# Performance work log

Hardware: AMD Instinct MI355X
Metric: run time of the kernel (lower is better)

The kernel has to match this reference:

```python
import jax, jax.numpy as jnp
import numpy as np

N = 150000   # total supergraph nodes (entities+events+chains)
D = 128      # embed_size
H = 4        # attention heads
DH = D // H  # head dim
E = 300000   # edges per layer
L = 4        # layer_specs length
A = 8        # edge attr dim
T = 10       # num_edge_type
TIME_SCALE = 24.0
SLOPE = 0.2  # negative_slope


def setup_inputs() -> dict:
    key = jax.random.key(0)
    ks = jax.random.split(key, 16)
    nrm = lambda k, s, sc=1.0: jax.random.normal(k, s, dtype=jnp.float32) * sc
    return {
        'x': nrm(ks[0], (N, D), 0.1),
        'Wq': nrm(ks[1], (L, D, D), D ** -0.5),
        'Wk': nrm(ks[2], (L, D, D), D ** -0.5),
        'Wv': nrm(ks[3], (L, D, D), D ** -0.5),
        'Wskip': nrm(ks[4], (L, D, D), D ** -0.5),
        'Wa': nrm(ks[5], (L, A, D), 0.1),
        'time_w': nrm(ks[6], (D,)),
        'time_b': nrm(ks[7], (D,), 0.1),
        'dist_w': nrm(ks[8], (D,)),
        'dist_b': nrm(ks[9], (D,), 0.1),
        'type_table': nrm(ks[10], (T, D), 0.1),
        'bn_gamma': jnp.ones((L, D), jnp.float32),
        'bn_beta': jnp.zeros((L, D), jnp.float32),
        'beta': jnp.full((L,), 0.5, jnp.float32),
        'edge_attr': jax.random.uniform(ks[11], (L, E, A), dtype=jnp.float32),
        'edge_dt': jax.random.uniform(ks[12], (L, E), dtype=jnp.float32) * TIME_SCALE,
        'edge_ds': jax.random.uniform(ks[13], (L, E), dtype=jnp.float32) * 10.0,
        'edge_index': jax.random.randint(ks[14], (L, 2, E), 0, N),
        'edge_type': jax.random.randint(ks[15], (L, E), 0, T),
    }


def _layer(x, Wq, Wk, Wv, Wskip, Wa, time_w, time_b, dist_w, dist_b,
           type_table, gamma, bvec, beta, attr, dt, ds, ei, et):
    n = x.shape[0]
    src, dst = ei[0], ei[1]
    # continuous time / distance encoders: cos basis (TimeEncoder / 'time' DistanceEncoder)
    te = jnp.cos((dt / TIME_SCALE)[:, None] * time_w + time_b)   # [E,D]
    de = jnp.cos(ds[:, None] * dist_w + dist_b)                  # [E,D]
    # 'add' edge/time fusion: attr MLP + time + dist + edge-type embeddings
    edge_feat = attr @ Wa + te + de + type_table[et]             # [E,D]
    kv_in = x[src] + edge_feat                                   # gather + fuse
    q = (x @ Wq).reshape(n, H, DH)[dst]                          # [E,H,DH]
    k = (kv_in @ Wk).reshape(-1, H, DH)
    v = (kv_in @ Wv).reshape(-1, H, DH)
    logits = (q * k).sum(-1) * (DH ** -0.5)                      # [E,H]
    logits = jnp.where(logits >= 0, logits, SLOPE * logits)      # leaky_relu(negative_slope)
    # segment softmax over incoming edges of each destination node
    m = jax.ops.segment_max(logits, dst, num_segments=n)
    a = jnp.exp(logits - m[dst])
    denom = jax.ops.segment_sum(a, dst, num_segments=n)
    a = a / denom[dst]
    agg = jax.ops.segment_sum(a[..., None] * v, dst, num_segments=n).reshape(n, D)
    # beta-weighted residual (learn_beta) with skip projection
    out = beta * (x @ Wskip) + (1.0 - beta) * agg
    # BatchNorm1d (training-mode batch stats) + ReLU
    mu = out.mean(0)
    var = out.var(0)
    out = (out - mu) * jax.lax.rsqrt(var + 1e-5) * gamma + bvec
    return jax.nn.relu(out)


def reference(x, Wq, Wk, Wv, Wskip, Wa, time_w, time_b, dist_w, dist_b,
              type_table, bn_gamma, bn_beta, beta, edge_attr, edge_dt,
              edge_ds, edge_index, edge_type):
    for l in range(L):  # entity2event, event2event, event2chain (time filter), chain2chain
        x = _layer(x, Wq[l], Wk[l], Wv[l], Wskip[l], Wa[l],
                   time_w, time_b, dist_w, dist_b, type_table,
                   bn_gamma[l], bn_beta[l], beta[l],
                   edge_attr[l], edge_dt[l], edge_ds[l],
                   edge_index[l], edge_type[l])
    return x
```

## Files before the change

### kernel.cpp

```cpp
#include <hip/hip_runtime.h>

typedef unsigned int u32;
typedef unsigned short u16;
typedef short bf16x8 __attribute__((ext_vector_type(8)));
typedef float f32x4 __attribute__((ext_vector_type(4)));

#define N_NODES 150000
#define E_EDGES 300000
#define L_CNT   151552
#define ETILES  9375
#define NTILES  4688
#define KVBLKS  37500
#define PREPB   42192
#define SCATB   2344

__device__ __forceinline__ float blo(u32 u){ return __uint_as_float(u << 16); }
__device__ __forceinline__ float bhi(u32 u){ return __uint_as_float(u & 0xffff0000u); }
__device__ __forceinline__ float b2f(u16 h){ return __uint_as_float(((u32)h) << 16); }
__device__ __forceinline__ u16 f2bf(float f){
  u32 u = __float_as_uint(f);
  return (u16)((u + 0x7fffu + ((u >> 16) & 1u)) >> 16);
}
__device__ __forceinline__ u32 pack2(float a, float b){
  return (u32)f2bf(a) | ((u32)f2bf(b) << 16);
}

__device__ __forceinline__ f32x4 mfma16(bf16x8 a, bf16x8 b, f32x4 c){
  return __builtin_amdgcn_mfma_f32_16x16x32_bf16(a, b, c, 0, 0, 0);
}

__device__ __forceinline__ int opsw(int r, int k){ return (r * 128 + k) ^ ((r & 7) << 3); }
__device__ __forceinline__ int csw(int r, int n){ return (r * 128 + n) ^ (((r >> 2) & 3) << 3); }

__global__ __launch_bounds__(256)
void k_wt(const float* __restrict__ Wq, const float* __restrict__ Wk,
          const float* __restrict__ Wv, const float* __restrict__ Ws,
          u16* __restrict__ Wt)
{
  const int m = blockIdx.x;
  const float* src = (m < 4 ? Wq : m < 8 ? Wk : m < 12 ? Wv : Ws)
                     + (size_t)(m & 3) * 16384;
  u16* dst = Wt + (size_t)m * 16384;
  const int t = threadIdx.x;
  for (int i = 0; i < 16; ++i) {
    int idx = i * 256 + t;
    int n = idx >> 5;
    int k4 = (idx & 31) << 2;
    ushort4 o;
    o.x = f2bf(src[(k4 + 0) * 128 + n]);
    o.y = f2bf(src[(k4 + 1) * 128 + n]);
    o.z = f2bf(src[(k4 + 2) * 128 + n]);
    o.w = f2bf(src[(k4 + 3) * 128 + n]);
    *(ushort4*)(dst + n * 128 + k4) = o;
  }
}


__global__ __launch_bounds__(256)
void k_hist(const int* __restrict__ eidx, int* __restrict__ counts)
{
  const int l = blockIdx.y;
  const int e = blockIdx.x * 256 + threadIdx.x;
  if (e < E_EDGES) {
    int dst = eidx[(size_t)l * 2 * E_EDGES + E_EDGES + e];
    atomicAdd(&counts[(size_t)l * L_CNT + dst], 1);
  }
}

__global__ __launch_bounds__(256)
void k_scan1(const int* __restrict__ counts, int* __restrict__ rowptr,
             int* __restrict__ bsum)
{
  __shared__ int sh[256];
  const int b = blockIdx.x, l = blockIdx.y;
  const int t = threadIdx.x;
  const int* c = counts + (size_t)l * L_CNT + b * 2048;
  int* rp = rowptr + (size_t)l * L_CNT + b * 2048;
  int v[8]; int s = 0;
  #pragma unroll
  for (int j = 0; j < 8; ++j) { v[j] = c[t * 8 + j]; s += v[j]; }
  sh[t] = s; __syncthreads();
  for (int off = 1; off < 256; off <<= 1) {
    int x = (t >= off) ? sh[t - off] : 0;
    __syncthreads();
    sh[t] += x;
    __syncthreads();
  }
  int excl = (t == 0) ? 0 : sh[t - 1];
  if (t == 255) bsum[l * 128 + b] = sh[255];
  int run = excl;
  #pragma unroll
  for (int j = 0; j < 8; ++j) { rp[t * 8 + j] = run; run += v[j]; }
}

__global__ __launch_bounds__(128)
void k_scan2(int* __restrict__ bsum)
{
  __shared__ int sh[128];
  const int l = blockIdx.x, t = threadIdx.x;
  int v = (t < 74) ? bsum[l * 128 + t] : 0;
  sh[t] = v; __syncthreads();
  for (int off = 1; off < 128; off <<= 1) {
    int x = (t >= off) ? sh[t - off] : 0;
    __syncthreads();
    sh[t] += x;
    __syncthreads();
  }
  int excl = (t == 0) ? 0 : sh[t - 1];
  if (t < 74) bsum[l * 128 + t] = excl;
}

__global__ __launch_bounds__(256)
void k_scan3(int* __restrict__ rowptr, int* __restrict__ tmp,
             const int* __restrict__ bsum)
{
  const int l = blockIdx.y;
  const int q = blockIdx.x * 256 + threadIdx.x;
  int v = rowptr[(size_t)l * L_CNT + q] + bsum[l * 128 + (q >> 11)];
  rowptr[(size_t)l * L_CNT + q] = v;
  tmp[(size_t)l * L_CNT + q] = v;
}

__device__ __forceinline__ void scatter_one(
    int e, const int* __restrict__ srcP, const int* __restrict__ dstP,
    const int* __restrict__ etP, const float* __restrict__ dtP,
    const float* __restrict__ dsP, const float* __restrict__ attrP,
    int* __restrict__ tmpL, u32* __restrict__ meta)
{
  int dst = dstP[e];
  int pos = atomicAdd(&tmpL[dst], 1);
  int src = srcP[e];
  int et  = etP[e];
  float dtn = dtP[e] * (1.0f / 24.0f);
  float dsv = dsP[e];
  float4 aA = *(const float4*)(attrP + (size_t)e * 8);
  float4 aB = *(const float4*)(attrP + (size_t)e * 8 + 4);
  uint4 r0, r1;
  r0.x = (u32)src;
  r0.y = (u32)dst | ((u32)et << 20);
  r0.z = __float_as_uint(dtn);
  r0.w = __float_as_uint(dsv);
  r1.x = pack2(aA.x, aA.y); r1.y = pack2(aA.z, aA.w);
  r1.z = pack2(aB.x, aB.y); r1.w = pack2(aB.z, aB.w);
  u32* mp = meta + (size_t)pos * 8;
  *(uint4*)mp = r0;
  *(uint4*)(mp + 4) = r1;
}

__global__ __launch_bounds__(256)
void k_scatter(const int* __restrict__ srcP, const int* __restrict__ dstP,
               const int* __restrict__ etP, const float* __restrict__ dtP,
               const float* __restrict__ dsP, const float* __restrict__ attrP,
               int* __restrict__ tmpL, u32* __restrict__ meta)
{
  const int e = blockIdx.x * 256 + threadIdx.x;
  if (e < E_EDGES)
    scatter_one(e, srcP, dstP, etP, dtP, dsP, attrP, tmpL, meta);
}

__global__ __launch_bounds__(128)
void bn_stats(const float* __restrict__ colsum, const float* __restrict__ colsumsq,
              const float* __restrict__ gamma, const float* __restrict__ bvec,
              float* __restrict__ scsh)
{
  const int d = threadIdx.x;
  const float invN = 1.f / 150000.f;
  float mu = colsum[d] * invN;
  float var = colsumsq[d] * invN - mu * mu;
  float sc = gamma[d] * rsqrtf(var + 1e-5f);
  scsh[d] = sc;
  scsh[128 + d] = bvec[d] - mu * sc;
}


template<int XF32, int BN>
__global__ __launch_bounds__(128, 2)
void prep(const void* __restrict__ xg, const u16* __restrict__ WtQ,
          const u16* __restrict__ WtS, const float* __restrict__ scsh,
          u16* __restrict__ Qo, u16* __restrict__ So,
          const float* __restrict__ Wa, const float* __restrict__ tw,
          const float* __restrict__ tb, const float* __restrict__ dw,
          const float* __restrict__ db, const float* __restrict__ ttab,
          const u32* __restrict__ meta, u16* __restrict__ kvV,
          const int* __restrict__ srcN, const int* __restrict__ dstN,
          const int* __restrict__ etN, const float* __restrict__ dtN,
          const float* __restrict__ dsN, const float* __restrict__ attrN,
          int* __restrict__ tmpN, u32* __restrict__ metaN)
{
  __shared__ __align__(16) u16 As[4160];
  __shared__ __align__(16) u16 Bs[4160];
  const int b = blockIdx.x;
  const int t = threadIdx.x;

  if (b >= PREPB) {
    int e = (b - PREPB) * 128 + t;
    if (metaN != nullptr && e < E_EDGES)
      scatter_one(e, srcN, dstN, etN, dtN, dsN, attrN, tmpN, metaN);
    return;
  }

  if (b % 9 == 0) {
    const int w = t >> 6, lane = t & 63;
    const int lr = lane & 15, hi = lane >> 4;
    const int row0 = (b / 9) * 32;
    const int nr = min(32, N_NODES - row0);
    const u16* Wt = w ? WtS : WtQ;
    u16* C = w ? So : Qo;

    bf16x8 wt[8][4];
    #pragma unroll
    for (int nb = 0; nb < 8; ++nb)
      #pragma unroll
      for (int ks = 0; ks < 4; ++ks)
        wt[nb][ks] = *(const bf16x8*)(Wt + (nb * 16 + lr) * 128 + ks * 32 + hi * 8);

    #pragma unroll
    for (int i = 0; i < 4; ++i) {
      int idx = i * 128 + t;
      int r = idx >> 4, c8 = (idx & 15) << 3;
      if (r < nr) {
        if (XF32) {
          float4 vA = *(const float4*)((const float*)xg + (size_t)(row0 + r) * 128 + c8);
          float4 vB = *(const float4*)((const float*)xg + (size_t)(row0 + r) * 128 + c8 + 4);
          uint4 o;
          o.x = pack2(vA.x, vA.y); o.y = pack2(vA.z, vA.w);
          o.z = pack2(vB.x, vB.y); o.w = pack2(vB.z, vB.w);
          *(uint4*)(As + opsw(r, c8)) = o;
        } else {
          uint4 v = *(const uint4*)((const u16*)xg + (size_t)(row0 + r) * 128 + c8);
          if (BN) {
            float4 scA = *(const float4*)(scsh + c8);
            float4 scB = *(const float4*)(scsh + c8 + 4);
            float4 shA = *(const float4*)(scsh + 128 + c8);
            float4 shB = *(const float4*)(scsh + 128 + c8 + 4);
            float e0v = fmaxf(fmaf(blo(v.x), scA.x, shA.x), 0.f);
            float e1v = fmaxf(fmaf(bhi(v.x), scA.y, shA.y), 0.f);
            float e2v = fmaxf(fmaf(blo(v.y), scA.z, shA.z), 0.f);
            float e3v = fmaxf(fmaf(bhi(v.y), scA.w, shA.w), 0.f);
            float e4v = fmaxf(fmaf(blo(v.z), scB.x, shB.x), 0.f);
            float e5v = fmaxf(fmaf(bhi(v.z), scB.y, shB.y), 0.f);
            float e6v = fmaxf(fmaf(blo(v.w), scB.z, shB.z), 0.f);
            float e7v = fmaxf(fmaf(bhi(v.w), scB.w, shB.w), 0.f);
            v.x = pack2(e0v, e1v); v.y = pack2(e2v, e3v);
            v.z = pack2(e4v, e5v); v.w = pack2(e6v, e7v);
          }
          *(uint4*)(As + opsw(r, c8)) = v;
        }
      } else {
        *(uint4*)(As + opsw(r, c8)) = make_uint4(0, 0, 0, 0);
      }
    }
    __syncthreads();

    f32x4 acc[2][8];
    #pragma unroll
    for (int a = 0; a < 2; ++a)
      #pragma unroll
      for (int bb = 0; bb < 8; ++bb) {
        acc[a][bb][0] = 0.f; acc[a][bb][1] = 0.f;
        acc[a][bb][2] = 0.f; acc[a][bb][3] = 0.f;
      }
    #pragma unroll
    for (int ks = 0; ks < 4; ++ks) {
      const int kb = ks * 32 + hi * 8;
      bf16x8 a0 = *(const bf16x8*)(As + opsw(lr, kb));
      bf16x8 a1 = *(const bf16x8*)(As + opsw(16 + lr, kb));
      #pragma unroll
      for (int nb = 0; nb < 8; ++nb) {
        acc[0][nb] = mfma16(a0, wt[nb][ks], acc[0][nb]);
        acc[1][nb] = mfma16(a1, wt[nb][ks], acc[1][nb]);
      }
    }
    __syncthreads();

    u16* Cs = w ? Bs : As;
    const int g4 = hi << 2;
    #pragma unroll
    for (int mt = 0; mt < 2; ++mt)
      #pragma unroll
      for (int nt = 0; nt < 8; ++nt)
        #pragma unroll
        for (int j = 0; j < 4; ++j)
          Cs[csw(mt * 16 + g4 + j, nt * 16 + lr)] = f2bf(acc[mt][nt][j]);
    #pragma unroll
    for (int i = 0; i < 8; ++i) {
      int idx = i * 64 + lane;
      int r = idx >> 4, n8 = (idx & 15) << 3;
      if (r < nr) {
        uint4 v = *(const uint4*)(Cs + csw(r, n8));
        *(uint4*)(C + (size_t)(row0 + r) * 128 + n8) = v;
      }
    }
  } else {
    const int blk = b - 1 - (b / 9);
    if (blk >= KVBLKS) return;
    const int idx = blk * 128 + t;
    const int e = idx >> 4;
    const int c8 = (idx & 15) << 3;
    const u32* mp = meta + (size_t)e * 8;
    uint4 m0 = *(const uint4*)mp;
    uint4 m1 = *(const uint4*)(mp + 4);
    const int src = (int)m0.x;
    const int et = (int)(m0.y >> 20);
    const float dtn = __uint_as_float(m0.z);
    const float dss = __uint_as_float(m0.w);
    float aa[8] = { blo(m1.x), bhi(m1.x), blo(m1.y), bhi(m1.y),
                    blo(m1.z), bhi(m1.z), blo(m1.w), bhi(m1.w) };
    const float4 twA = *(const float4*)(tw + c8);
    const float4 twB = *(const float4*)(tw + c8 + 4);
    const float4 tbA = *(const float4*)(tb + c8);
    const float4 tbB = *(const float4*)(tb + c8 + 4);
    const float4 dwA = *(const float4*)(dw + c8);
    const float4 dwB = *(const float4*)(dw + c8 + 4);
    const float4 dbA = *(const float4*)(db + c8);
    const float4 dbB = *(const float4*)(db + c8 + 4);
    const float4 ttA = *(const float4*)(ttab + et * 128 + c8);
    const float4 ttB = *(const float4*)(ttab + et * 128 + c8 + 4);
    float f[8];
    f[0] = __cosf(fmaf(dtn, twA.x, tbA.x)) + __cosf(fmaf(dss, dwA.x, dbA.x)) + ttA.x;
    f[1] = __cosf(fmaf(dtn, twA.y, tbA.y)) + __cosf(fmaf(dss, dwA.y, dbA.y)) + ttA.y;
    f[2] = __cosf(fmaf(dtn, twA.z, tbA.z)) + __cosf(fmaf(dss, dwA.z, dbA.z)) + ttA.z;
    f[3] = __cosf(fmaf(dtn, twA.w, tbA.w)) + __cosf(fmaf(dss, dwA.w, dbA.w)) + ttA.w;
    f[4] = __cosf(fmaf(dtn, twB.x, tbB.x)) + __cosf(fmaf(dss, dwB.x, dbB.x)) + ttB.x;
    f[5] = __cosf(fmaf(dtn, twB.y, tbB.y)) + __cosf(fmaf(dss, dwB.y, dbB.y)) + ttB.y;
    f[6] = __cosf(fmaf(dtn, twB.z, tbB.z)) + __cosf(fmaf(dss, dwB.z, dbB.z)) + ttB.z;
    f[7] = __cosf(fmaf(dtn, twB.w, tbB.w)) + __cosf(fmaf(dss, dwB.w, dbB.w)) + ttB.w;
    #pragma unroll
    for (int a = 0; a < 8; ++a) {
      float4 wA = *(const float4*)(Wa + a * 128 + c8);
      float4 wB = *(const float4*)(Wa + a * 128 + c8 + 4);
      f[0] = fmaf(aa[a], wA.x, f[0]);
      f[1] = fmaf(aa[a], wA.y, f[1]);
      f[2] = fmaf(aa[a], wA.z, f[2]);
      f[3] = fmaf(aa[a], wA.w, f[3]);
      f[4] = fmaf(aa[a], wB.x, f[4]);
      f[5] = fmaf(aa[a], wB.y, f[5]);
      f[6] = fmaf(aa[a], wB.z, f[6]);
      f[7] = fmaf(aa[a], wB.w, f[7]);
    }
    float xv[8];
    if (XF32) {
      float4 xA = *(const float4*)((const float*)xg + (size_t)src * 128 + c8);
      float4 xB = *(const float4*)((const float*)xg + (size_t)src * 128 + c8 + 4);
      xv[0] = xA.x; xv[1] = xA.y; xv[2] = xA.z; xv[3] = xA.w;
      xv[4] = xB.x; xv[5] = xB.y; xv[6] = xB.z; xv[7] = xB.w;
    } else {
      uint4 xr = *(const uint4*)((const u16*)xg + (size_t)src * 128 + c8);
      xv[0] = blo(xr.x); xv[1] = bhi(xr.x); xv[2] = blo(xr.y); xv[3] = bhi(xr.y);
      xv[4] = blo(xr.z); xv[5] = bhi(xr.z); xv[6] = blo(xr.w); xv[7] = bhi(xr.w);
    }
    if (BN) {
      float4 scA = *(const float4*)(scsh + c8);
      float4 scB = *(const float4*)(scsh + c8 + 4);
      float4 shA = *(const float4*)(scsh + 128 + c8);
      float4 shB = *(const float4*)(scsh + 128 + c8 + 4);
      xv[0] = fmaxf(fmaf(xv[0], scA.x, shA.x), 0.f);
      xv[1] = fmaxf(fmaf(xv[1], scA.y, shA.y), 0.f);
      xv[2] = fmaxf(fmaf(xv[2], scA.z, shA.z), 0.f);
      xv[3] = fmaxf(fmaf(xv[3], scA.w, shA.w), 0.f);
      xv[4] = fmaxf(fmaf(xv[4], scB.x, shB.x), 0.f);
      xv[5] = fmaxf(fmaf(xv[5], scB.y, shB.y), 0.f);
      xv[6] = fmaxf(fmaf(xv[6], scB.z, shB.z), 0.f);
      xv[7] = fmaxf(fmaf(xv[7], scB.w, shB.w), 0.f);
    }
    uint4 o;
    o.x = pack2(xv[0] + f[0], xv[1] + f[1]);
    o.y = pack2(xv[2] + f[2], xv[3] + f[3]);
    o.z = pack2(xv[4] + f[4], xv[5] + f[5]);
    o.w = pack2(xv[6] + f[6], xv[7] + f[7]);
    *(uint4*)(kvV + (size_t)e * 128 + c8) = o;
  }
}


__global__ __launch_bounds__(128, 2)
void edge_kv(const u16* __restrict__ WtK, const u16* __restrict__ WtV,
             const u32* __restrict__ meta, const u16* __restrict__ Qb,
             u16* __restrict__ kvV, float* __restrict__ logits)
{
  __shared__ __align__(16) u16 KVs[4160];
  __shared__ __align__(16) u16 Qs[4160];
  __shared__ int dstSh[32];
  const int t = threadIdx.x;
  const int w = t >> 6, lane = t & 63;
  const int lr = lane & 15, hi = lane >> 4;
  const int e0 = blockIdx.x * 32;
  const u16* Wt = w ? WtV : WtK;

  bf16x8 wt[8][4];
  #pragma unroll
  for (int nb = 0; nb < 8; ++nb)
    #pragma unroll
    for (int ks = 0; ks < 4; ++ks)
      wt[nb][ks] = *(const bf16x8*)(Wt + (nb * 16 + lr) * 128 + ks * 32 + hi * 8);

  if (w == 0) {
    #pragma unroll
    for (int i = 0; i < 8; ++i) {
      int idx = i * 64 + lane;
      int r = idx >> 4, c8 = (idx & 15) << 3;
      uint4 v = *(const uint4*)(kvV + (size_t)(e0 + r) * 128 + c8);
      *(uint4*)(KVs + opsw(r, c8)) = v;
    }
  } else {
    if (lane < 32)
      dstSh[lane] = (int)(meta[(size_t)(e0 + lane) * 8 + 1] & 0xFFFFFu);
    #pragma unroll
    for (int i = 0; i < 8; ++i) {
      int idx = i * 64 + lane;
      int r = idx >> 4, c8 = (idx & 15) << 3;
      int qrow = dstSh[r];
      uint4 qv = *(const uint4*)(Qb + (size_t)qrow * 128 + c8);
      *(uint4*)(Qs + opsw(r, c8)) = qv;
    }
  }
  __syncthreads();

  if (w == 0) {
    #pragma unroll
    for (int eb = 0; eb < 2; ++eb) {
      f32x4 kacc[8];
      #pragma unroll
      for (int b = 0; b < 8; ++b) {
        kacc[b][0] = 0.f; kacc[b][1] = 0.f; kacc[b][2] = 0.f; kacc[b][3] = 0.f;
      }
      #pragma unroll
      for (int ks = 0; ks < 4; ++ks) {
        bf16x8 ef = *(const bf16x8*)(KVs + opsw(eb * 16 + lr, ks * 32 + hi * 8));
        #pragma unroll
        for (int nb = 0; nb < 8; ++nb)
          kacc[nb] = mfma16(wt[nb][ks], ef, kacc[nb]);
      }
      const int el = eb * 16 + lr;
      float hs[4] = {0.f, 0.f, 0.f, 0.f};
      #pragma unroll
      for (int nb = 0; nb < 8; ++nb) {
        ushort4 q = *(const ushort4*)(Qs + opsw(el, nb * 16 + hi * 4));
        hs[nb >> 1] += b2f(q.x) * kacc[nb][0] + b2f(q.y) * kacc[nb][1]
                     + b2f(q.z) * kacc[nb][2] + b2f(q.w) * kacc[nb][3];
      }
      #pragma unroll
      for (int h = 0; h < 4; ++h) {
        hs[h] += __shfl_xor(hs[h], 16, 64);
        hs[h] += __shfl_xor(hs[h], 32, 64);
        hs[h] *= 0.17677669529663687f;
        hs[h] = (hs[h] >= 0.f) ? hs[h] : 0.2f * hs[h];
      }
      if (lane < 16)
        *(float4*)(logits + (size_t)(e0 + el) * 4) = make_float4(hs[0], hs[1], hs[2], hs[3]);
    }
    __syncthreads();
  } else {
    f32x4 vacc[2][8];
    #pragma unroll
    for (int a = 0; a < 2; ++a)
      #pragma unroll
      for (int b = 0; b < 8; ++b) {
        vacc[a][b][0] = 0.f; vacc[a][b][1] = 0.f;
        vacc[a][b][2] = 0.f; vacc[a][b][3] = 0.f;
      }
    #pragma unroll
    for (int ks = 0; ks < 4; ++ks) {
      const int kb = ks * 32 + hi * 8;
      bf16x8 a0 = *(const bf16x8*)(KVs + opsw(lr, kb));
      bf16x8 a1 = *(const bf16x8*)(KVs + opsw(16 + lr, kb));
      #pragma unroll
      for (int nb = 0; nb < 8; ++nb) {
        vacc[0][nb] = mfma16(a0, wt[nb][ks], vacc[0][nb]);
        vacc[1][nb] = mfma16(a1, wt[nb][ks], vacc[1][nb]);
      }
    }
    __syncthreads();
    const int g4 = hi << 2;
    #pragma unroll
    for (int mt = 0; mt < 2; ++mt)
      #pragma unroll
      for (int nt = 0; nt < 8; ++nt)
        #pragma unroll
        for (int j = 0; j < 4; ++j)
          Qs[csw(mt * 16 + g4 + j, nt * 16 + lr)] = f2bf(vacc[mt][nt][j]);
    #pragma unroll
    for (int i = 0; i < 8; ++i) {
      int idx = i * 64 + lane;
      int r = idx >> 4, n8 = (idx & 15) << 3;
      uint4 v = *(const uint4*)(Qs + csw(r, n8));
      *(uint4*)(kvV + (size_t)(e0 + r) * 128 + n8) = v;
    }
  }
}

template<int PREBF16>
__global__ __launch_bounds__(256)
void node_agg(const u16* __restrict__ Vs, const float* __restrict__ logits,
              const int* __restrict__ rowptr, const u16* __restrict__ S,
              const float* __restrict__ betaP, float* __restrict__ pre,
              u16* __restrict__ preb, float* __restrict__ colsum,
              float* __restrict__ colsumsq)
{
  __shared__ float red[1024];
  const int t = threadIdx.x;
  const int g = t >> 5;
  const int lane = t & 31;
  const int d0 = lane * 4;
  const int h = lane >> 3;
  const float beta = *betaP;
  const float omb = 1.f - beta;
  float s4[4] = {0.f, 0.f, 0.f, 0.f};
  float q4[4] = {0.f, 0.f, 0.f, 0.f};
  for (int rep = 0; rep < 16; ++rep) {
    int n = blockIdx.x * 128 + rep * 8 + g;
    if (n < N_NODES) {
      int rs = rowptr[n], re = rowptr[n + 1];
      float m = -1e30f;
      for (int i = rs; i < re; ++i)
        m = fmaxf(m, logits[(size_t)i * 4 + h]);
      float den = 0.f;
      float a0 = 0.f, a1 = 0.f, a2 = 0.f, a3 = 0.f;
      for (int i = rs; i < re; ++i) {
        float wgt = __expf(logits[(size_t)i * 4 + h] - m);
        den += wgt;
        ushort4 v = *(const ushort4*)(Vs + (size_t)i * 128 + d0);
        a0 = fmaf(wgt, b2f(v.x), a0);
        a1 = fmaf(wgt, b2f(v.y), a1);
        a2 = fmaf(wgt, b2f(v.z), a2);
        a3 = fmaf(wgt, b2f(v.w), a3);
      }
      float inv = (den > 0.f) ? (omb / den) : 0.f;
      ushort4 sv = *(const ushort4*)(S + (size_t)n * 128 + d0);
      float p0 = fmaf(beta, b2f(sv.x), a0 * inv);
      float p1 = fmaf(beta, b2f(sv.y), a1 * inv);
      float p2 = fmaf(beta, b2f(sv.z), a2 * inv);
      float p3 = fmaf(beta, b2f(sv.w), a3 * inv);
      if (PREBF16) {
        ushort4 o;
        o.x = f2bf(p0); o.y = f2bf(p1); o.z = f2bf(p2); o.w = f2bf(p3);
        *(ushort4*)(preb + (size_t)n * 128 + d0) = o;
      } else {
        *(float4*)(pre + (size_t)n * 128 + d0) = make_float4(p0, p1, p2, p3);
      }
      s4[0] += p0; s4[1] += p1; s4[2] += p2; s4[3] += p3;
      q4[0] += p0 * p0; q4[1] += p1 * p1; q4[2] += p2 * p2; q4[3] += p3 * p3;
    }
  }
  *(float4*)(&red[g * 128 + d0]) = make_float4(s4[0], s4[1], s4[2], s4[3]);
  __syncthreads();
  if (t < 128) {
    float tot = 0.f;
    #pragma unroll
    for (int gg = 0; gg < 8; ++gg) tot += red[gg * 128 + t];
    atomicAdd(&colsum[t], tot);
  }
  __syncthreads();
  *(float4*)(&red[g * 128 + d0]) = make_float4(q4[0], q4[1], q4[2], q4[3]);
  __syncthreads();
  if (t < 128) {
    float tot = 0.f;
    #pragma unroll
    for (int gg = 0; gg < 8; ++gg) tot += red[gg * 128 + t];
    atomicAdd(&colsumsq[t], tot);
  }
}

__global__ __launch_bounds__(256)
void bn_apply(const float* __restrict__ pre, const float* __restrict__ colsum,
              const float* __restrict__ colsumsq, const float* __restrict__ gamma,
              const float* __restrict__ bvec, float* __restrict__ outf)
{
  const int idx = blockIdx.x * 256 + threadIdx.x;
  const int n = idx >> 5;
  const int d0 = (idx & 31) * 4;
  const float invN = 1.f / 150000.f;
  float4 p = *(const float4*)(pre + (size_t)n * 128 + d0);
  float4 cs = *(const float4*)(colsum + d0);
  float4 cq = *(const float4*)(colsumsq + d0);
  float4 gm = *(const float4*)(gamma + d0);
  float4 bv = *(const float4*)(bvec + d0);
  float mu, var, y;
  mu = cs.x * invN; var = cq.x * invN - mu * mu;
  y = (p.x - mu) * rsqrtf(var + 1e-5f) * gm.x + bv.x; p.x = fmaxf(y, 0.f);
  mu = cs.y * invN; var = cq.y * invN - mu * mu;
  y = (p.y - mu) * rsqrtf(var + 1e-5f) * gm.y + bv.y; p.y = fmaxf(y, 0.f);
  mu = cs.z * invN; var = cq.z * invN - mu * mu;
  y = (p.z - mu) * rsqrtf(var + 1e-5f) * gm.z + bv.z; p.z = fmaxf(y, 0.f);
  mu = cs.w * invN; var = cq.w * invN - mu * mu;
  y = (p.w - mu) * rsqrtf(var + 1e-5f) * gm.w + bv.w; p.w = fmaxf(y, 0.f);
  *(float4*)(outf + (size_t)n * 128 + d0) = p;
}

extern "C" void kernel_launch(void* const* d_in, const int* in_sizes, int n_in,
                              void* d_out, int out_size, void* d_ws, size_t ws_size,
                              hipStream_t stream)
{
  const float* x0    = (const float*)d_in[0];
  const float* Wq    = (const float*)d_in[1];
  const float* Wk    = (const float*)d_in[2];
  const float* Wv    = (const float*)d_in[3];
  const float* Wsk   = (const float*)d_in[4];
  const float* Wa    = (const float*)d_in[5];
  const float* tw    = (const float*)d_in[6];
  const float* tb    = (const float*)d_in[7];
  const float* dw    = (const float*)d_in[8];
  const float* db    = (const float*)d_in[9];
  const float* ttab  = (const float*)d_in[10];
  const float* gam   = (const float*)d_in[11];
  const float* bet   = (const float*)d_in[12];
  const float* betaP = (const float*)d_in[13];
  const float* attr  = (const float*)d_in[14];
  const float* dt    = (const float*)d_in[15];
  const float* dsv   = (const float*)d_in[16];
  const int*   eidx  = (const int*)d_in[17];
  const int*   etyp  = (const int*)d_in[18];

  char* p = (char*)d_ws;
  u16* xbf  = (u16*)p;       p += 38400000;
  u16* Q    = (u16*)p;       p += 38400000;
  u16* S    = (u16*)p;       p += 38400000;
  u16* kvV  = (u16*)p;       p += 76800000;
  float* logits = (float*)p; p += 4800000;
  int* rowptr = (int*)p;     p += 4 * L_CNT * 4;
  int* tmp    = (int*)p;     p += 4 * L_CNT * 4;
  int* bsum   = (int*)p;     p += 4 * 128 * 4;
  float* colsum   = (float*)p; p += 512;
  float* colsumsq = (float*)p; p += 512;
  float* scsh     = (float*)p; p += 1024;
  u16* Wt = (u16*)p;         p += 16 * 16384 * 2;
  u32* metaA = (u32*)p;      p += (size_t)E_EDGES * 32;
  u32* metaB = (u32*)p;      p += (size_t)E_EDGES * 32;

  float* pre = (float*)d_out;

  k_wt<<<16, 256, 0, stream>>>(Wq, Wk, Wv, Wsk, Wt);
  hipMemsetAsync(tmp, 0, 4 * L_CNT * 4, stream);
  k_hist<<<dim3(1172, 4), 256, 0, stream>>>(eidx, tmp);
  k_scan1<<<dim3(74, 4), 256, 0, stream>>>(tmp, rowptr, bsum);
  k_scan2<<<4, 128, 0, stream>>>(bsum);
  k_scan3<<<dim3(592, 4), 256, 0, stream>>>(rowptr, tmp, bsum);
  k_scatter<<<1172, 256, 0, stream>>>(
      eidx, eidx + 300000, etyp, dt, dsv, attr, tmp, metaA);

  for (int l = 0; l < 4; ++l) {
    const int* rpl = rowptr + (size_t)l * L_CNT;
    const u16* WtQl = Wt + (size_t)l * 16384;
    const u16* WtKl = Wt + (size_t)(4 + l) * 16384;
    const u16* WtVl = Wt + (size_t)(8 + l) * 16384;
    const u16* WtSl = Wt + (size_t)(12 + l) * 16384;
    const float* Wal = Wa + (size_t)l * 1024;
    u32* metaCur = (l & 1) ? metaB : metaA;
    u32* metaNxt = (l & 1) ? metaA : metaB;
    const int ln = l + 1;
    const int* srcN = eidx + (size_t)ln * 600000;
    const int* dstN = srcN + 300000;

    hipMemsetAsync(colsum, 0, 1024, stream);

    const int prepGrid = PREPB + ((l < 3) ? SCATB : 0);
    if (l == 0) {
      prep<1, 0><<<prepGrid, 128, 0, stream>>>(
          (const void*)x0, WtQl, WtSl, scsh, Q, S,
          Wal, tw, tb, dw, db, ttab, metaCur, kvV,
          srcN, dstN, etyp + (size_t)ln * 300000, dt + (size_t)ln * 300000,
          dsv + (size_t)ln * 300000, attr + (size_t)ln * 2400000,
          tmp + (size_t)ln * L_CNT, metaNxt);
    } else if (l < 3) {
      prep<0, 1><<<prepGrid, 128, 0, stream>>>(
          (const void*)xbf, WtQl, WtSl, scsh, Q, S,
          Wal, tw, tb, dw, db, ttab, metaCur, kvV,
          srcN, dstN, etyp + (size_t)ln * 300000, dt + (size_t)ln * 300000,
          dsv + (size_t)ln * 300000, attr + (size_t)ln * 2400000,
          tmp + (size_t)ln * L_CNT, metaNxt);
    } else {
      prep<0, 1><<<prepGrid, 128, 0, stream>>>(
          (const void*)xbf, WtQl, WtSl, scsh, Q, S,
          Wal, tw, tb, dw, db, ttab, metaCur, kvV,
          nullptr, nullptr, nullptr, nullptr, nullptr, nullptr,
          nullptr, nullptr);
    }

    edge_kv<<<ETILES, 128, 0, stream>>>(WtKl, WtVl, metaCur, Q, kvV, logits);

    if (l < 3) {
      node_agg<1><<<1172, 256, 0, stream>>>(kvV, logits, rpl, S, betaP + l,
                                            nullptr, xbf, colsum, colsumsq);
      bn_stats<<<1, 128, 0, stream>>>(colsum, colsumsq, gam + (size_t)l * 128,
                                      bet + (size_t)l * 128, scsh);
    } else {
      node_agg<0><<<1172, 256, 0, stream>>>(kvV, logits, rpl, S, betaP + l,
                                            pre, nullptr, colsum, colsumsq);
      bn_apply<<<18750, 256, 0, stream>>>(pre, colsum, colsumsq,
                                          gam + (size_t)l * 128,
                                          bet + (size_t)l * 128, (float*)d_out);
    }
  }
}
```

Measured before the change: 1.438 ms.

## Move next-layer edge scatter from prep kernel into node_agg tail blocks

The per-edge metadata scatter for the next layer now runs as extra blocks appended to the node_agg launch instead of the prep launch. Prep drops its interleaved 1-in-9 block mapping and uses a plain split: node-GEMM tiles first, then edge blocks. The aim is to overlap the memory-bound scatter with the latency-bound, irregular aggregation kernel rather than with the compute-heavy prep, and to simplify prep's block mapping. The cost is that node_agg carries extra parameters, and its scatter blocks compete with aggregation work for bandwidth.

```diff
diff --git a/kernel.cpp b/kernel.cpp
--- a/kernel.cpp
+++ b/kernel.cpp
@@ -11,8 +11,8 @@
 #define ETILES  9375
 #define NTILES  4688
 #define KVBLKS  37500
-#define PREPB   42192
-#define SCATB   2344
+#define AGGB    1172
+#define SCATB   1172
 
 __device__ __forceinline__ float blo(u32 u){ return __uint_as_float(u << 16); }
 __device__ __forceinline__ float bhi(u32 u){ return __uint_as_float(u & 0xffff0000u); }
@@ -181,28 +181,16 @@
           const float* __restrict__ Wa, const float* __restrict__ tw,
           const float* __restrict__ tb, const float* __restrict__ dw,
           const float* __restrict__ db, const float* __restrict__ ttab,
-          const u32* __restrict__ meta, u16* __restrict__ kvV,
-          const int* __restrict__ srcN, const int* __restrict__ dstN,
-          const int* __restrict__ etN, const float* __restrict__ dtN,
-          const float* __restrict__ dsN, const float* __restrict__ attrN,
-          int* __restrict__ tmpN, u32* __restrict__ metaN)
+          const u32* __restrict__ meta, u16* __restrict__ kvV)
 {
   __shared__ __align__(16) u16 As[4160];
   __shared__ __align__(16) u16 Bs[4160];
-  const int b = blockIdx.x;
   const int t = threadIdx.x;
 
-  if (b >= PREPB) {
-    int e = (b - PREPB) * 128 + t;
-    if (metaN != nullptr && e < E_EDGES)
-      scatter_one(e, srcN, dstN, etN, dtN, dsN, attrN, tmpN, metaN);
-    return;
-  }
-
-  if (b % 9 == 0) {
+  if (blockIdx.x < NTILES) {
     const int w = t >> 6, lane = t & 63;
     const int lr = lane & 15, hi = lane >> 4;
-    const int row0 = (b / 9) * 32;
+    const int row0 = blockIdx.x * 32;
     const int nr = min(32, N_NODES - row0);
     const u16* Wt = w ? WtS : WtQ;
     u16* C = w ? So : Qo;
@@ -256,9 +244,9 @@
     #pragma unroll
     for (int a = 0; a < 2; ++a)
       #pragma unroll
-      for (int bb = 0; bb < 8; ++bb) {
-        acc[a][bb][0] = 0.f; acc[a][bb][1] = 0.f;
-        acc[a][bb][2] = 0.f; acc[a][bb][3] = 0.f;
+      for (int b = 0; b < 8; ++b) {
+        acc[a][b][0] = 0.f; acc[a][b][1] = 0.f;
+        acc[a][b][2] = 0.f; acc[a][b][3] = 0.f;
       }
     #pragma unroll
     for (int ks = 0; ks < 4; ++ks) {
@@ -292,9 +280,7 @@
       }
     }
   } else {
-    const int blk = b - 1 - (b / 9);
-    if (blk >= KVBLKS) return;
-    const int idx = blk * 128 + t;
+    const int idx = (blockIdx.x - NTILES) * 128 + t;
     const int e = idx >> 4;
     const int c8 = (idx & 15) << 3;
     const u32* mp = meta + (size_t)e * 8;
@@ -495,8 +481,19 @@
               const int* __restrict__ rowptr, const u16* __restrict__ S,
               const float* __restrict__ betaP, float* __restrict__ pre,
               u16* __restrict__ preb, float* __restrict__ colsum,
-              float* __restrict__ colsumsq)
-{
+              float* __restrict__ colsumsq,
+              const int* __restrict__ srcN, const int* __restrict__ dstN,
+              const int* __restrict__ etN, const float* __restrict__ dtN,
+              const float* __restrict__ dsN, const float* __restrict__ attrN,
+              int* __restrict__ tmpN, u32* __restrict__ metaN)
+{
+  if (blockIdx.x >= AGGB) {
+    int e = (int)(blockIdx.x - AGGB) * 256 + threadIdx.x;
+    if (metaN != nullptr && e < E_EDGES)
+      scatter_one(e, srcN, dstN, etN, dtN, dsN, attrN, tmpN, metaN);
+    return;
+  }
+
   __shared__ float red[1024];
   const int t = threadIdx.x;
   const int g = t >> 5;
@@ -635,7 +632,7 @@
   k_scan1<<<dim3(74, 4), 256, 0, stream>>>(tmp, rowptr, bsum);
   k_scan2<<<4, 128, 0, stream>>>(bsum);
   k_scan3<<<dim3(592, 4), 256, 0, stream>>>(rowptr, tmp, bsum);
-  k_scatter<<<1172, 256, 0, stream>>>(
+  k_scatter<<<SCATB, 256, 0, stream>>>(
       eidx, eidx + 300000, etyp, dt, dsv, attr, tmp, metaA);
 
   for (int l = 0; l < 4; ++l) {
@@ -653,39 +650,31 @@
 
     hipMemsetAsync(colsum, 0, 1024, stream);
 
-    const int prepGrid = PREPB + ((l < 3) ? SCATB : 0);
     if (l == 0) {
-      prep<1, 0><<<prepGrid, 128, 0, stream>>>(
+      prep<1, 0><<<NTILES + KVBLKS, 128, 0, stream>>>(
           (const void*)x0, WtQl, WtSl, scsh, Q, S,
-          Wal, tw, tb, dw, db, ttab, metaCur, kvV,
+          Wal, tw, tb, dw, db, ttab, metaCur, kvV);
+    } else {
+      prep<0, 1><<<NTILES + KVBLKS, 128, 0, stream>>>(
+          (const void*)xbf, WtQl, WtSl, scsh, Q, S,
+          Wal, tw, tb, dw, db, ttab, metaCur, kvV);
+    }
+
+    edge_kv<<<ETILES, 128, 0, stream>>>(WtKl, WtVl, metaCur, Q, kvV, logits);
+
+    if (l < 3) {
+      node_agg<1><<<AGGB + SCATB, 256, 0, stream>>>(
+          kvV, logits, rpl, S, betaP + l, nullptr, xbf, colsum, colsumsq,
           srcN, dstN, etyp + (size_t)ln * 300000, dt + (size_t)ln * 300000,
           dsv + (size_t)ln * 300000, attr + (size_t)ln * 2400000,
           tmp + (size_t)ln * L_CNT, metaNxt);
-    } else if (l < 3) {
-      prep<0, 1><<<prepGrid, 128, 0, stream>>>(
-          (const void*)xbf, WtQl, WtSl, scsh, Q, S,
-          Wal, tw, tb, dw, db, ttab, metaCur, kvV,
-          srcN, dstN, etyp + (size_t)ln * 300000, dt + (size_t)ln * 300000,
-          dsv + (size_t)ln * 300000, attr + (size_t)ln * 2400000,
-          tmp + (size_t)ln * L_CNT, metaNxt);
-    } else {
-      prep<0, 1><<<prepGrid, 128, 0, stream>>>(
-          (const void*)xbf, WtQl, WtSl, scsh, Q, S,
-          Wal, tw, tb, dw, db, ttab, metaCur, kvV,
-          nullptr, nullptr, nullptr, nullptr, nullptr, nullptr,
-          nullptr, nullptr);
-    }
-
-    edge_kv<<<ETILES, 128, 0, stream>>>(WtKl, WtVl, metaCur, Q, kvV, logits);
-
-    if (l < 3) {
-      node_agg<1><<<1172, 256, 0, stream>>>(kvV, logits, rpl, S, betaP + l,
-                                            nullptr, xbf, colsum, colsumsq);
       bn_stats<<<1, 128, 0, stream>>>(colsum, colsumsq, gam + (size_t)l * 128,
                                       bet + (size_t)l * 128, scsh);
     } else {
-      node_agg<0><<<1172, 256, 0, stream>>>(kvV, logits, rpl, S, betaP + l,
-                                            pre, nullptr, colsum, colsumsq);
+      node_agg<0><<<AGGB, 256, 0, stream>>>(
+          kvV, logits, rpl, S, betaP + l, pre, nullptr, colsum, colsumsq,
+          nullptr, nullptr, nullptr, nullptr, nullptr, nullptr,
+          nullptr, nullptr);
       bn_apply<<<18750, 256, 0, stream>>>(pre, colsum, colsumsq,
                                           gam + (size_t)l * 128,
                                           bet + (size_t)l * 128, (float*)d_out);
```

Result: no change. 1.415 ms (median of 2 runs) (-1.6%).
